# Optimization experiments

Measured on AMD Instinct MI355X. Metric: run time of the kernel, lower is better.

## Reference

```python
import jax, jax.numpy as jnp
import numpy as np

B, S, H = 16, 1024, 768


def setup_inputs() -> dict:
    key = jax.random.key(0)
    ks = jax.random.split(key, 12)
    s = 1.0 / np.sqrt(H)
    return {
        "encoder_outputs": jax.random.normal(ks[0], (B, S, H), dtype=jnp.float32),
        "mask": jax.random.randint(ks[1], (B, S), 0, 2, dtype=jnp.int32),
        "Wq": jax.random.uniform(ks[2], (H, H), jnp.float32, -s, s),
        "bq": jnp.zeros((H,), jnp.float32),
        "Wk": jax.random.uniform(ks[3], (H, H), jnp.float32, -s, s),
        "bk": jnp.zeros((H,), jnp.float32),
        "Wv": jax.random.uniform(ks[4], (H, H), jnp.float32, -s, s),
        "bv": jnp.zeros((H,), jnp.float32),
        "W1": jax.random.uniform(ks[5], (H, H), jnp.float32, -s, s),
        "b1": jnp.zeros((H,), jnp.float32),
        "W2": jax.random.uniform(ks[6], (H, H), jnp.float32, -s, s),
        "b2": jnp.zeros((H,), jnp.float32),
    }


def reference(encoder_outputs, mask, Wq, bq, Wk, bk, Wv, bv, W1, b1, W2, b2):
    x = encoder_outputs  # [B, S, H]
    inv_sqrt_h = 1.0 / jnp.sqrt(jnp.asarray(H, x.dtype))
    # ReLU-gated query/key projections (dropout=0 -> identity)
    q = jax.nn.relu(jnp.einsum('bsh,oh->bso', x, Wq) + bq)
    k = jax.nn.relu(jnp.einsum('bsh,oh->bso', x, Wk) + bk)
    score = jnp.einsum('bsh,bth->bst', q, k) * inv_sqrt_h  # [B, S, S]
    v = jnp.einsum('bsh,oh->bso', x, Wv) + bv
    m = mask.astype(x.dtype)  # [B, S]
    new_mask = m[:, :, None] * m[:, None, :]  # outer product [B, S, S]
    score = score - (1.0 - new_mask) * 1e12
    w = jax.nn.softmax(score, axis=2) * new_mask
    out = jnp.einsum('bst,bth->bsh', w, v)
    # FFN residual
    h1 = jax.nn.relu(jnp.einsum('bsh,oh->bso', out, W1) + b1)
    out = jnp.einsum('bsh,oh->bso', h1, W2) + b2 + out
    return out
```

## Files before the change

kernel.cpp:

```cpp
#include <hip/hip_runtime.h>
#include <hip/hip_bf16.h>

typedef __bf16 bf16_t;
typedef __bf16 bf16x8 __attribute__((ext_vector_type(8)));
typedef __bf16 bf16x4 __attribute__((ext_vector_type(4)));
typedef float f32x4 __attribute__((ext_vector_type(4)));
typedef unsigned int u32;
typedef const __attribute__((address_space(1))) u32* gptr_t;
typedef __attribute__((address_space(3))) u32* lptr_t;

static constexpr int Bb = 16, Ss = 1024, Hh = 768;

__global__ __launch_bounds__(256) void compact_mask(
    const int* __restrict__ mask, int* __restrict__ tok, int* __restrict__ cnt)
{
    const int b = blockIdx.x;
    const int t = threadIdx.x;
    const int4 m4 = *(const int4*)&mask[(b << 10) + (t << 2)];
    const int c = (m4.x != 0) + (m4.y != 0) + (m4.z != 0) + (m4.w != 0);
    __shared__ int sb[256];
    sb[t] = c;
    __syncthreads();
    for (int off = 1; off < 256; off <<= 1) {
        int v = (t >= off) ? sb[t - off] : 0;
        __syncthreads();
        sb[t] += v;
        __syncthreads();
    }
    int p = sb[t] - c;
    int* tb = tok + (b << 10);
    if (m4.x) tb[p++] = (t << 2) + 0;
    if (m4.y) tb[p++] = (t << 2) + 1;
    if (m4.z) tb[p++] = (t << 2) + 2;
    if (m4.w) tb[p++] = (t << 2) + 3;
    if (t == 255) cnt[b] = sb[255];
}

__global__ __launch_bounds__(256) void cvt_all(
    const float* __restrict__ x,
    const float* __restrict__ w0, const float* __restrict__ w1,
    const float* __restrict__ w2, const float* __restrict__ w3,
    const float* __restrict__ w4,
    const float* __restrict__ bq, const float* __restrict__ bk,
    const float* __restrict__ bv,
    const float* __restrict__ b1, const float* __restrict__ b2,
    const int* __restrict__ tok, const int* __restrict__ cnt,
    bf16_t* __restrict__ xc, bf16_t* __restrict__ wdst, float* __restrict__ bdst,
    float* __restrict__ cvec)
{
    const int bx = blockIdx.x;
    const int t = threadIdx.x;
    if (bx < 2880) {
        int seg = bx / 576;
        const float* src = seg == 0 ? w0 : seg == 1 ? w1 : seg == 2 ? w2 : seg == 3 ? w3 : w4;
        int i = (bx % 576) * 256 + t;
        float4 v = ((const float4*)src)[i];
        bf16x4 o = { (bf16_t)v.x, (bf16_t)v.y, (bf16_t)v.z, (bf16_t)v.w };
        ((bf16x4*)(wdst + (long)seg * 589824))[i] = o;
    } else if (bx < 2889) {
        int i = (bx - 2880) * 256 + t;
        if (i < 2304)
            bdst[i] = i < 768 ? bq[i] : i < 1536 ? bk[i - 768] : bv[i - 1536];
    } else if (bx < 19273) {
        const int idx = bx - 2889;
        const int b = idx >> 10, j = idx & 1023;
        if (j < cnt[b] && t < 192) {
            const int s = tok[(b << 10) + j];
            float4 v = ((const float4*)(x + ((long)((b << 10) + s)) * 768))[t];
            bf16x4 o = { (bf16_t)v.x, (bf16_t)v.y, (bf16_t)v.z, (bf16_t)v.w };
            ((bf16x4*)(xc + ((long)((b << 10) + j)) * 768))[t] = o;
        }
    } else {
        const int o = ((bx - 19273) << 3) + (t >> 5);
        const int l = t & 31;
        const float* wr = w4 + (long)o * 768;
        float acc = 0.f;
        for (int h = l; h < 768; h += 32) acc += wr[h] * fmaxf(b1[h], 0.f);
#pragma unroll
        for (int off = 16; off; off >>= 1) acc += __shfl_down(acc, off, 32);
        if (l == 0) cvec[o] = acc + b2[o];
    }
}

__device__ __forceinline__ void async_cp16(const void* g, void* l)
{
    __builtin_amdgcn_global_load_lds((gptr_t)g, (lptr_t)l, 16, 0, 0);
}

enum { EG_QKV = 0, EG_SCORE_C = 1, EG_PV = 2, EG_FFN1 = 3, EG_FFN2 = 4 };

#define SBAR __builtin_amdgcn_s_barrier()
#define VMW(n) asm volatile("s_waitcnt vmcnt(" #n ")" ::: "memory")

template <int EPI, int BM, int BN>
__global__ __launch_bounds__(512) void mfma_gemm(
    const bf16_t* __restrict__ A, const bf16_t* __restrict__ B,
    const float* __restrict__ bias, const bf16_t* __restrict__ resid,
    const int* __restrict__ tok, const int* __restrict__ cnt,
    void* __restrict__ Cout, bf16_t* __restrict__ out2, bf16_t* __restrict__ out3,
    int K, int lda, int ldb, long sA, long sB, float scale)
{
    const int gx = gridDim.x, gy = gridDim.y;
    const int nwg = gx * gy * gridDim.z;
    int lid = blockIdx.x + gx * (blockIdx.y + gy * blockIdx.z);
    lid = (lid & 7) * (nwg >> 3) + (lid >> 3);
    const int bxs = lid % gx;
    const int tmp = lid / gx;
    const int bys = tmp % gy;
    const int bz  = tmp / gy;

    const int cb = cnt[bz];
    const int m0 = bys * BM;
    const int n0 = bxs * BN;
    if (m0 >= cb) return;
    if constexpr (EPI == EG_SCORE_C) { if (n0 >= cb) return; }
    const int Kend = (EPI == EG_PV) ? ((cb + 31) & ~31) : K;
    const int nk = Kend >> 5;

    constexpr int MI = 2, NI = 4;
    constexpr int ASZ = BM * 32, BSZ = BN * 32;
    constexpr int NB = 3;

    __shared__ __align__(16) bf16_t Asl[NB * ASZ];
    __shared__ __align__(16) bf16_t Bsl[NB * BSZ];

    const int tid = threadIdx.x;
    const int wid = tid >> 6;
    const int lane = tid & 63;
    const int wm = wid & 3, wn = wid >> 2;

    const bf16_t* Ab = A + (long)bz * sA;
    const bf16_t* Bp = B + (long)bz * sB;

    const int srow = (wid << 4) + (lane >> 2);
    const int scol = ((lane & 3) ^ ((lane >> 3) & 3)) << 3;

    const bf16_t* pa0 = Ab + (long)(m0 + srow) * lda + scol;
    const bf16_t* pb0 = Bp + (long)(n0 + srow) * ldb + scol;

    const int woff = wid << 9;

    const int frag_off = ((lane & 15) << 5) + (((lane >> 4) ^ ((lane >> 1) & 3)) << 3);

    auto stage = [&](int kk, int buf) {
        async_cp16(pa0 + kk, &Asl[buf * ASZ + woff]);
        async_cp16(pb0 + kk, &Bsl[buf * BSZ + woff]);
    };

    f32x4 acc[MI][NI] = {};

    stage(0, 0);
    if (nk > 1) stage(32, 1);
    __builtin_amdgcn_sched_barrier(0);
    if (nk > 1) { VMW(2); } else { VMW(0); }
    SBAR;

    int cur = 0;
    for (int it = 0; it < nk; ++it) {
        if (it + 2 < nk) {
            int tgt = cur + 2; if (tgt >= NB) tgt -= NB;
            stage((it + 2) << 5, tgt);
        }

        const int cba = cur * ASZ, cbb = cur * BSZ;
        bf16x8 af[MI], bfr[NI];
#pragma unroll
        for (int i = 0; i < MI; i++)
            af[i] = *(const bf16x8*)&Asl[cba + ((wm * MI + i) << 9) + frag_off];
#pragma unroll
        for (int j = 0; j < NI; j++)
            bfr[j] = *(const bf16x8*)&Bsl[cbb + ((wn * NI + j) << 9) + frag_off];
#pragma unroll
        for (int i = 0; i < MI; i++)
#pragma unroll
            for (int j = 0; j < NI; j++)
                acc[i][j] = __builtin_amdgcn_mfma_f32_16x16x32_bf16(af[i], bfr[j], acc[i][j], 0, 0, 0);

        __builtin_amdgcn_sched_barrier(0);
        if (it + 1 < nk) {
            if (it + 2 < nk) { VMW(2); } else { VMW(0); }
            SBAR;
        }
        cur = (cur + 1 == NB) ? 0 : cur + 1;
    }

    const int mb_ = m0 + wm * 32;
    const int nb_ = n0 + wn * 64;
    const int colw = lane & 15;
    const int rowq = (lane >> 4) << 2;

    if constexpr (EPI == EG_QKV) {
        float bj[NI];
#pragma unroll
        for (int j = 0; j < NI; j++) bj[j] = bias[nb_ + (j << 4) + colw];
        if (nb_ < 1536) {
            bf16_t* C = ((nb_ < 768) ? (bf16_t*)Cout : out2) + (long)bz * 786432;
            const int cbase = (nb_ < 768) ? nb_ : nb_ - 768;
#pragma unroll
            for (int i = 0; i < MI; i++)
#pragma unroll
                for (int j = 0; j < NI; j++)
#pragma unroll
                    for (int r = 0; r < 4; r++) {
                        int row = mb_ + (i << 4) + rowq + r;
                        int col = cbase + (j << 4) + colw;
                        C[(long)row * Hh + col] = (bf16_t)fmaxf(acc[i][j][r] + bj[j], 0.f);
                    }
        } else {
            bf16_t* C = out3 + (long)bz * 786432;
#pragma unroll
            for (int i = 0; i < MI; i++) {
                const int jc0 = mb_ + (i << 4) + rowq;
#pragma unroll
                for (int j = 0; j < NI; j++) {
                    const int col = nb_ - 1536 + (j << 4) + colw;
                    bf16x4 o = { (bf16_t)(acc[i][j][0] + bj[j]), (bf16_t)(acc[i][j][1] + bj[j]),
                                 (bf16_t)(acc[i][j][2] + bj[j]), (bf16_t)(acc[i][j][3] + bj[j]) };
                    *(bf16x4*)&C[(long)col * 1024 + jc0] = o;
                }
            }
        }
    } else if constexpr (EPI == EG_SCORE_C) {
        bf16_t* C = (bf16_t*)Cout + (long)bz * 1048576;
#pragma unroll
        for (int i = 0; i < MI; i++) {
            const int kbase = mb_ + (i << 4) + rowq;
#pragma unroll
            for (int j = 0; j < NI; j++) {
                const int qrow = nb_ + (j << 4) + colw;
                bf16x4 o = { (bf16_t)(acc[i][j][0] * scale), (bf16_t)(acc[i][j][1] * scale),
                             (bf16_t)(acc[i][j][2] * scale), (bf16_t)(acc[i][j][3] * scale) };
                *(bf16x4*)&C[(long)qrow * 1024 + kbase] = o;
            }
        }
    } else if constexpr (EPI == EG_FFN2) {
        float* outp = (float*)Cout;
        const bf16_t* crow = resid + (long)bz * 786432;
        const int* tb = tok + (bz << 10);
        float bj[NI];
#pragma unroll
        for (int j = 0; j < NI; j++) bj[j] = bias[nb_ + (j << 4) + colw];
#pragma unroll
        for (int i = 0; i < MI; i++)
#pragma unroll
            for (int r = 0; r < 4; r++) {
                const int jq = mb_ + (i << 4) + rowq + r;
                if (jq < cb) {
                    const int s = tb[jq];
                    float* orow = outp + ((long)((bz << 10) + s)) * 768;
                    const bf16_t* cr = crow + (long)jq * 768;
#pragma unroll
                    for (int j = 0; j < NI; j++) {
                        const int col = nb_ + (j << 4) + colw;
                        orow[col] = acc[i][j][r] + bj[j] + (float)cr[col];
                    }
                }
            }
    } else {
        bf16_t* C = (bf16_t*)Cout + (long)bz * 786432;
        float bj[NI];
#pragma unroll
        for (int j = 0; j < NI; j++) bj[j] = 0.f;
        if constexpr (EPI == EG_FFN1) {
#pragma unroll
            for (int j = 0; j < NI; j++) bj[j] = bias[nb_ + (j << 4) + colw];
        }
#pragma unroll
        for (int i = 0; i < MI; i++)
#pragma unroll
            for (int j = 0; j < NI; j++)
#pragma unroll
                for (int r = 0; r < 4; r++) {
                    int row = mb_ + (i << 4) + rowq + r;
                    int col = nb_ + (j << 4) + colw;
                    float v = acc[i][j][r] + bj[j];
                    if constexpr (EPI == EG_FFN1) v = fmaxf(v, 0.f);
                    C[(long)row * Hh + col] = (bf16_t)v;
                }
    }
}

__global__ __launch_bounds__(256) void softmax_rows(
    bf16_t* __restrict__ S_, const int* __restrict__ cnt,
    const int* __restrict__ mask, const float* __restrict__ cvec,
    float* __restrict__ out)
{
    const int b = blockIdx.y;
    const int t = threadIdx.x;

    if (blockIdx.z == 1) {
        const int s = blockIdx.x;
        if (t >= 192 || mask[(b << 10) + s]) return;
        float4 v = ((const float4*)cvec)[t];
        ((float4*)(out + ((long)((b << 10) + s)) * 768))[t] = v;
        return;
    }

    const int jq = blockIdx.x;
    const int cb = cnt[b];
    if (jq >= cb) return;
    bf16_t* p = S_ + (((long)(b << 10)) + jq) * 1024;
    const int t0 = t << 2;

    bf16x4 v4 = *(const bf16x4*)&p[t0];
    float v0 = (t0 + 0 < cb) ? (float)v4[0] : -1e30f;
    float v1 = (t0 + 1 < cb) ? (float)v4[1] : -1e30f;
    float v2 = (t0 + 2 < cb) ? (float)v4[2] : -1e30f;
    float v3 = (t0 + 3 < cb) ? (float)v4[3] : -1e30f;

    float mx = fmaxf(fmaxf(v0, v1), fmaxf(v2, v3));
#pragma unroll
    for (int off = 32; off; off >>= 1) mx = fmaxf(mx, __shfl_down(mx, off, 64));
    __shared__ float redm[4], reds[4];
    if ((t & 63) == 0) redm[t >> 6] = mx;
    __syncthreads();
    mx = fmaxf(fmaxf(redm[0], redm[1]), fmaxf(redm[2], redm[3]));

    float e0 = __expf(v0 - mx), e1 = __expf(v1 - mx);
    float e2 = __expf(v2 - mx), e3 = __expf(v3 - mx);
    float sm = e0 + e1 + e2 + e3;
#pragma unroll
    for (int off = 32; off; off >>= 1) sm += __shfl_down(sm, off, 64);
    if ((t & 63) == 0) reds[t >> 6] = sm;
    __syncthreads();
    sm = reds[0] + reds[1] + reds[2] + reds[3];

    const float inv = 1.f / sm;
    bf16x4 o = { (bf16_t)(e0 * inv), (bf16_t)(e1 * inv),
                 (bf16_t)(e2 * inv), (bf16_t)(e3 * inv) };
    *(bf16x4*)&p[t0] = o;
}

extern "C" void kernel_launch(void* const* d_in, const int* in_sizes, int n_in,
                              void* d_out, int out_size, void* d_ws, size_t ws_size,
                              hipStream_t stream)
{
    const float* x  = (const float*)d_in[0];
    const int* mask = (const int*)d_in[1];
    const float* Wq = (const float*)d_in[2];
    const float* bq = (const float*)d_in[3];
    const float* Wk = (const float*)d_in[4];
    const float* bk = (const float*)d_in[5];
    const float* Wv = (const float*)d_in[6];
    const float* bv = (const float*)d_in[7];
    const float* W1 = (const float*)d_in[8];
    const float* b1 = (const float*)d_in[9];
    const float* W2 = (const float*)d_in[10];
    const float* b2 = (const float*)d_in[11];
    float* out = (float*)d_out;

    char* w = (char*)d_ws;
    bf16_t* xc   = (bf16_t*)(w + 0);
    bf16_t* qc   = (bf16_t*)(w + 25165824);
    bf16_t* kc   = (bf16_t*)(w + 50331648);
    bf16_t* vTc  = (bf16_t*)(w + 75497472);
    bf16_t* sc   = (bf16_t*)(w + 100663296);
    bf16_t* wqkv = (bf16_t*)(w + 134217728);
    bf16_t* w1b  = (bf16_t*)(w + 137756672);
    bf16_t* w2b  = (bf16_t*)(w + 138936320);
    float*  bqkv = (float*) (w + 140115968);
    int*    tok  = (int*)   (w + 140125184);
    int*    cnt  = (int*)   (w + 140190720);
    float*  cvec = (float*) (w + 140190784);
    bf16_t* ctxc = xc;
    bf16_t* h1c  = qc;

    const float inv_sqrt_h = 0.036084391824351615f;
    dim3 blk(256);
    dim3 blk8(512);

    compact_mask<<<16, blk, 0, stream>>>(mask, tok, cnt);
    cvt_all<<<19369, blk, 0, stream>>>(x, Wq, Wk, Wv, W1, W2, bq, bk, bv, b1, b2,
                                       tok, cnt, xc, wqkv, bqkv, cvec);

    mfma_gemm<EG_QKV, 128, 128><<<dim3(18, 8, 16), blk8, 0, stream>>>(
        xc, wqkv, bqkv, nullptr, tok, cnt, qc, kc, vTc,
        768, 768, 768, 786432, 0, 1.f);

    mfma_gemm<EG_SCORE_C, 128, 128><<<dim3(8, 8, 16), blk8, 0, stream>>>(
        kc, qc, nullptr, nullptr, tok, cnt, sc, nullptr, nullptr,
        768, 768, 768, 786432, 786432, inv_sqrt_h);

    softmax_rows<<<dim3(1024, 16, 2), blk, 0, stream>>>(sc, cnt, mask, cvec, out);

    mfma_gemm<EG_PV, 128, 128><<<dim3(6, 8, 16), blk8, 0, stream>>>(
        sc, vTc, nullptr, nullptr, tok, cnt, ctxc, nullptr, nullptr,
        0, 1024, 1024, 1048576, 786432, 1.f);

    mfma_gemm<EG_FFN1, 128, 128><<<dim3(6, 8, 16), blk8, 0, stream>>>(
        ctxc, w1b, b1, nullptr, tok, cnt, h1c, nullptr, nullptr,
        768, 768, 768, 786432, 0, 1.f);

    mfma_gemm<EG_FFN2, 128, 128><<<dim3(6, 8, 16), blk8, 0, stream>>>(
        h1c, w2b, b2, ctxc, tok, cnt, out, nullptr, nullptr,
        768, 768, 768, 786432, 0, 1.f);
}
```

Before: 282.2 us.

## Load A fragments directly from global into registers, double-buffer B in LDS

The GEMM main loop stops staging the A tile through LDS. Each wave now loads its A MFMA fragments straight from global memory into registers, ping-ponging between two register sets, while only B goes through a two-buffer LDS ring (down from three). The aim is to cut LDS traffic and footprint and raise occupancy. In exchange the A loads are less coalesced, the prefetch is shallower, and each step waits on all outstanding loads with VMW(0), which may expose global latency.

```diff
diff --git a/kernel.cpp b/kernel.cpp
--- a/kernel.cpp
+++ b/kernel.cpp
@@ -118,11 +118,9 @@
     const int nk = Kend >> 5;
 
     constexpr int MI = 2, NI = 4;
-    constexpr int ASZ = BM * 32, BSZ = BN * 32;
-    constexpr int NB = 3;
-
-    __shared__ __align__(16) bf16_t Asl[NB * ASZ];
-    __shared__ __align__(16) bf16_t Bsl[NB * BSZ];
+    constexpr int BSZ = BN * 32;
+
+    __shared__ __align__(16) bf16_t Bsl[2 * BSZ];
 
     const int tid = threadIdx.x;
     const int wid = tid >> 6;
@@ -134,54 +132,65 @@
 
     const int srow = (wid << 4) + (lane >> 2);
     const int scol = ((lane & 3) ^ ((lane >> 3) & 3)) << 3;
-
-    const bf16_t* pa0 = Ab + (long)(m0 + srow) * lda + scol;
     const bf16_t* pb0 = Bp + (long)(n0 + srow) * ldb + scol;
-
     const int woff = wid << 9;
 
     const int frag_off = ((lane & 15) << 5) + (((lane >> 4) ^ ((lane >> 1) & 3)) << 3);
 
-    auto stage = [&](int kk, int buf) {
-        async_cp16(pa0 + kk, &Asl[buf * ASZ + woff]);
-        async_cp16(pb0 + kk, &Bsl[buf * BSZ + woff]);
+    const int arow = lane & 15;
+    const int akc = (lane >> 4) << 3;
+    const bf16_t* pA0 = Ab + (long)(m0 + wm * 32 + arow) * lda + akc;
+    const bf16_t* pA1 = Ab + (long)(m0 + wm * 32 + 16 + arow) * lda + akc;
+
+    f32x4 acc[MI][NI] = {};
+    bf16x8 aA[MI], aB[MI], bfr[NI];
+
+    auto prefA = [&](int t, bf16x8* dst) {
+        dst[0] = *(const bf16x8*)(pA0 + ((long)t << 5));
+        dst[1] = *(const bf16x8*)(pA1 + ((long)t << 5));
     };
-
-    f32x4 acc[MI][NI] = {};
-
-    stage(0, 0);
-    if (nk > 1) stage(32, 1);
+    auto stageB = [&](int t, int buf) {
+        async_cp16(pb0 + (t << 5), &Bsl[buf * BSZ + woff]);
+    };
+    auto readB = [&](int buf) {
+#pragma unroll
+        for (int j = 0; j < NI; j++)
+            bfr[j] = *(const bf16x8*)&Bsl[buf * BSZ + ((wn * NI + j) << 9) + frag_off];
+    };
+    auto mfma8 = [&](const bf16x8* av) {
+#pragma unroll
+        for (int i = 0; i < MI; i++)
+#pragma unroll
+            for (int j = 0; j < NI; j++)
+                acc[i][j] = __builtin_amdgcn_mfma_f32_16x16x32_bf16(av[i], bfr[j], acc[i][j], 0, 0, 0);
+    };
+
+    prefA(0, aA);
+    stageB(0, 0);
     __builtin_amdgcn_sched_barrier(0);
-    if (nk > 1) { VMW(2); } else { VMW(0); }
-    SBAR;
-
-    int cur = 0;
-    for (int it = 0; it < nk; ++it) {
-        if (it + 2 < nk) {
-            int tgt = cur + 2; if (tgt >= NB) tgt -= NB;
-            stage((it + 2) << 5, tgt);
-        }
-
-        const int cba = cur * ASZ, cbb = cur * BSZ;
-        bf16x8 af[MI], bfr[NI];
-#pragma unroll
-        for (int i = 0; i < MI; i++)
-            af[i] = *(const bf16x8*)&Asl[cba + ((wm * MI + i) << 9) + frag_off];
-#pragma unroll
-        for (int j = 0; j < NI; j++)
-            bfr[j] = *(const bf16x8*)&Bsl[cbb + ((wn * NI + j) << 9) + frag_off];
-#pragma unroll
-        for (int i = 0; i < MI; i++)
-#pragma unroll
-            for (int j = 0; j < NI; j++)
-                acc[i][j] = __builtin_amdgcn_mfma_f32_16x16x32_bf16(af[i], bfr[j], acc[i][j], 0, 0, 0);
-
+    VMW(0); SBAR;
+
+    const int nkE = nk & ~1;
+    for (int it = 0; it < nkE; it += 2) {
+        prefA(it + 1, aB);
+        stageB(it + 1, 1);
+        readB(0);
         __builtin_amdgcn_sched_barrier(0);
-        if (it + 1 < nk) {
-            if (it + 2 < nk) { VMW(2); } else { VMW(0); }
-            SBAR;
-        }
-        cur = (cur + 1 == NB) ? 0 : cur + 1;
+        mfma8(aA);
+        __builtin_amdgcn_sched_barrier(0);
+        VMW(0); SBAR;
+
+        const bool m2 = (it + 2) < nk;
+        if (m2) { prefA(it + 2, aA); stageB(it + 2, 0); }
+        readB(1);
+        __builtin_amdgcn_sched_barrier(0);
+        mfma8(aB);
+        if (m2) { __builtin_amdgcn_sched_barrier(0); VMW(0); SBAR; }
+    }
+    if (nk & 1) {
+        readB(0);
+        __builtin_amdgcn_sched_barrier(0);
+        mfma8(aA);
     }
 
     const int mb_ = m0 + wm * 32;
```

Result: slower. 364.0 us (+29.0%).

## Switch GEMM mainloop to BK=64 double buffering with new LDS swizzle

Applied to the files above, without the earlier changes.

The generic GEMM mainloop now stages 64-wide K tiles into two LDS buffers instead of 32-wide tiles into a triple buffer. The global-to-LDS copy layout and fragment addressing use an 8-way XOR swizzle over the wider rows, each thread issues two copies per matrix per stage, and the PV path rounds K up to 64. This halves the number of barriers and waits per unit of K and gives each iteration twice as many MFMAs. The cost is shallower prefetch (one tile ahead, with a full vmcnt wait each iteration), more LDS per block, and extra padded work in PV when the masked count is not a multiple of 64.

```diff
diff --git a/kernel.cpp b/kernel.cpp
--- a/kernel.cpp
+++ b/kernel.cpp
@@ -114,15 +114,14 @@
     const int n0 = bxs * BN;
     if (m0 >= cb) return;
     if constexpr (EPI == EG_SCORE_C) { if (n0 >= cb) return; }
-    const int Kend = (EPI == EG_PV) ? ((cb + 31) & ~31) : K;
-    const int nk = Kend >> 5;
+    const int Kend = (EPI == EG_PV) ? ((cb + 63) & ~63) : K;
+    const int nk = Kend >> 6;
 
     constexpr int MI = 2, NI = 4;
-    constexpr int ASZ = BM * 32, BSZ = BN * 32;
-    constexpr int NB = 3;
-
-    __shared__ __align__(16) bf16_t Asl[NB * ASZ];
-    __shared__ __align__(16) bf16_t Bsl[NB * BSZ];
+    constexpr int TSZ = 128 * 64;
+
+    __shared__ __align__(16) bf16_t Asl[2 * TSZ];
+    __shared__ __align__(16) bf16_t Bsl[2 * TSZ];
 
     const int tid = threadIdx.x;
     const int wid = tid >> 6;
@@ -132,56 +131,66 @@
     const bf16_t* Ab = A + (long)bz * sA;
     const bf16_t* Bp = B + (long)bz * sB;
 
-    const int srow = (wid << 4) + (lane >> 2);
-    const int scol = ((lane & 3) ^ ((lane >> 3) & 3)) << 3;
-
-    const bf16_t* pa0 = Ab + (long)(m0 + srow) * lda + scol;
-    const bf16_t* pb0 = Bp + (long)(n0 + srow) * ldb + scol;
-
-    const int woff = wid << 9;
-
-    const int frag_off = ((lane & 15) << 5) + (((lane >> 4) ^ ((lane >> 1) & 3)) << 3);
-
-    auto stage = [&](int kk, int buf) {
-        async_cp16(pa0 + kk, &Asl[buf * ASZ + woff]);
-        async_cp16(pb0 + kk, &Bsl[buf * BSZ + woff]);
+    const int srow8 = lane >> 3;
+    const int scg = ((lane & 7) ^ srow8) << 3;
+
+    const bf16_t* pa[2];
+    const bf16_t* pb[2];
+#pragma unroll
+    for (int q = 0; q < 2; q++) {
+        pa[q] = Ab + (long)(m0 + (wid << 4) + (q << 3) + srow8) * lda + scg;
+        pb[q] = Bp + (long)(n0 + (wid << 4) + (q << 3) + srow8) * ldb + scg;
+    }
+    const int wrow = wid << 4;
+
+    const int arow = lane & 15;
+    const int axr = lane & 7;
+    const int f0 = (arow << 6) + (((lane >> 4)      ^ axr) << 3);
+    const int f1 = (arow << 6) + ((((lane >> 4) + 4) ^ axr) << 3);
+
+    auto stage = [&](int tk, int buf) {
+        const long ko = (long)tk << 6;
+#pragma unroll
+        for (int q = 0; q < 2; q++) {
+            async_cp16(pa[q] + ko, &Asl[buf * TSZ + ((wrow + (q << 3)) << 6)]);
+            async_cp16(pb[q] + ko, &Bsl[buf * TSZ + ((wrow + (q << 3)) << 6)]);
+        }
     };
 
     f32x4 acc[MI][NI] = {};
 
     stage(0, 0);
-    if (nk > 1) stage(32, 1);
     __builtin_amdgcn_sched_barrier(0);
-    if (nk > 1) { VMW(2); } else { VMW(0); }
-    SBAR;
-
-    int cur = 0;
-    for (int it = 0; it < nk; ++it) {
-        if (it + 2 < nk) {
-            int tgt = cur + 2; if (tgt >= NB) tgt -= NB;
-            stage((it + 2) << 5, tgt);
-        }
-
-        const int cba = cur * ASZ, cbb = cur * BSZ;
-        bf16x8 af[MI], bfr[NI];
-#pragma unroll
-        for (int i = 0; i < MI; i++)
-            af[i] = *(const bf16x8*)&Asl[cba + ((wm * MI + i) << 9) + frag_off];
-#pragma unroll
-        for (int j = 0; j < NI; j++)
-            bfr[j] = *(const bf16x8*)&Bsl[cbb + ((wn * NI + j) << 9) + frag_off];
-#pragma unroll
-        for (int i = 0; i < MI; i++)
-#pragma unroll
-            for (int j = 0; j < NI; j++)
-                acc[i][j] = __builtin_amdgcn_mfma_f32_16x16x32_bf16(af[i], bfr[j], acc[i][j], 0, 0, 0);
-
+    VMW(0); SBAR;
+
+    for (int t = 0; t < nk; ++t) {
+        if (t + 1 < nk) stage(t + 1, (t + 1) & 1);
+
+        const int cba = (t & 1) * TSZ;
+        bf16x8 af[MI][2], bfr[NI][2];
+#pragma unroll
+        for (int i = 0; i < MI; i++) {
+            const int rb = cba + ((wm * MI + i) << 10);
+            af[i][0] = *(const bf16x8*)&Asl[rb + f0];
+            af[i][1] = *(const bf16x8*)&Asl[rb + f1];
+        }
+#pragma unroll
+        for (int j = 0; j < NI; j++) {
+            const int rb = cba + ((wn * NI + j) << 10);
+            bfr[j][0] = *(const bf16x8*)&Bsl[rb + f0];
+            bfr[j][1] = *(const bf16x8*)&Bsl[rb + f1];
+        }
         __builtin_amdgcn_sched_barrier(0);
-        if (it + 1 < nk) {
-            if (it + 2 < nk) { VMW(2); } else { VMW(0); }
-            SBAR;
-        }
-        cur = (cur + 1 == NB) ? 0 : cur + 1;
+#pragma unroll
+        for (int kk = 0; kk < 2; kk++)
+#pragma unroll
+            for (int i = 0; i < MI; i++)
+#pragma unroll
+                for (int j = 0; j < NI; j++)
+                    acc[i][j] = __builtin_amdgcn_mfma_f32_16x16x32_bf16(
+                        af[i][kk], bfr[j][kk], acc[i][j], 0, 0, 0);
+        __builtin_amdgcn_sched_barrier(0);
+        if (t + 1 < nk) { VMW(0); SBAR; }
     }
 
     const int mb_ = m0 + wm * 32;
```

New measurement: 273.8 us. 3.0% less time.
